# Kernel tuning notes

Hardware: AMD Instinct MI355X
Metric: run time of the kernel (lower is better)

The kernel has to match this reference:

```python
import jax, jax.numpy as jnp
import numpy as np

N_SAMPLES = 131072
N_FRAMES = 128
CPD = 16
WINDOW = 1024
N_VOICES = 8
N_BLOCKS = 3
N_CP = 512
N_VERBS = 8
MAX_ACTIVE = 32
BASE_RES = 0.5
MAX_GAIN = 5.0
B = 4
E = 16


def fft_convolve(a, b):
    # linear convolution via zero-padded rFFT, truncated to input length
    n = a.shape[-1]
    fa = jnp.fft.rfft(a, n=2 * n, axis=-1)
    fb = jnp.fft.rfft(b, n=2 * n, axis=-1)
    return jnp.fft.irfft(fa * fb, n=2 * n, axis=-1)[..., :n]


def sparsify(x, k):
    # keep top-k entries of the whole control plane, zero the rest
    flat = x.reshape(-1)
    vals, idx = jax.lax.top_k(flat, k)
    return jnp.zeros_like(flat).at[idx].set(vals).reshape(x.shape)


def run_layer(cp, w1, decays, w2, audio_map, gains):
    # cp: [CPD, F]
    frames = cp.shape[-1]
    x = w1 @ cp
    orig = x
    logd = jnp.log(1e-12 + decays)  # [CPD]
    env = jnp.exp(jnp.cumsum(jnp.broadcast_to(logd[:, None], (CPD, frames)), axis=-1))
    x = fft_convolve(x, env)
    x = w2 @ x + orig
    cp_out = jnp.tanh(x * gains[:, None])
    audio = (audio_map @ cp_out).T.reshape(-1)  # [F*WINDOW], frame-major
    return audio, cp_out


def stack_forward(cp, w1s, w2s, audios, decays_p, gains_p, mix):
    wc = cp
    outs = []
    for i in range(N_BLOCKS):
        d = BASE_RES + jax.nn.sigmoid(decays_p[i]) * (1.0 - BASE_RES)
        g = jax.nn.sigmoid(gains_p[i]) * MAX_GAIN
        out, wc = run_layer(jax.nn.relu(wc), w1s[i], d, w2s[i], audios[i], g)
        outs.append(out)
    channels = jnp.stack(outs, axis=0)  # [N_BLOCKS, N_SAMPLES]
    mixed = jnp.einsum('ct,c->t', channels, jax.nn.softmax(mix))
    return mixed / (jnp.max(jnp.abs(mixed)) + 1e-8)  # max_norm


def event_forward(voice_l, cp_choice, amp, room_l, room_mix_l, times,
                  cp_items, verbs, w1, w2, audio_maps, decays, gains, mix):
    vidx = jnp.argmax(voice_l)  # hard voice one-hot (normalize=True -> value 1.0)
    cp = cp_items[jnp.argmax(cp_choice)].reshape(CPD, N_FRAMES)
    cp = sparsify(cp / (cp.sum() + 1e-8), MAX_ACTIVE)
    samples = stack_forward(cp, w1[vidx], w2[vidx], audio_maps[vidx],
                            decays[vidx], gains[vidx], mix[vidx])  # [N_SAMPLES]
    verb = verbs[jnp.argmax(room_l)]  # hard reverb lookup
    wet = fft_convolve(verb, samples)
    vm = jax.nn.softmax(room_mix_l)  # [wet, dry]
    final = wet * vm[0] + samples * vm[1]
    final = final * jnp.abs(amp[0])
    # DiracScheduler: upsample-with-holes then FFT convolve
    step = N_SAMPLES // N_FRAMES
    impulse = jnp.zeros(N_SAMPLES, final.dtype).at[jnp.arange(N_FRAMES) * step].set(times)
    return fft_convolve(final, impulse)


def setup_inputs():
    key = jax.random.key(0)
    ks = jax.random.split(key, 14)
    return {
        'voice': jax.random.normal(ks[0], (B, E, N_VOICES), jnp.float32),
        'control_plane_choice': jax.random.normal(ks[1], (B, E, N_CP), jnp.float32),
        'amplitudes': jax.random.uniform(ks[2], (B, E, 1), jnp.float32),
        'room_choice': jax.random.normal(ks[3], (B, E, N_VERBS), jnp.float32),
        'room_mix': jax.random.normal(ks[4], (B, E, 2), jnp.float32),
        'times': jax.random.uniform(ks[5], (B, E, N_FRAMES), jnp.float32),
        'cp_items': jax.random.uniform(ks[6], (N_CP, N_FRAMES * CPD), jnp.float32),
        'verbs': jax.random.normal(ks[7], (N_VERBS, N_SAMPLES), jnp.float32) * 0.01,
        'w1': jax.random.normal(ks[8], (N_VOICES, N_BLOCKS, CPD, CPD), jnp.float32) * 0.01,
        'w2': jax.random.normal(ks[9], (N_VOICES, N_BLOCKS, CPD, CPD), jnp.float32) * 0.01,
        'audio_maps': jax.random.normal(ks[10], (N_VOICES, N_BLOCKS, WINDOW, CPD), jnp.float32) * 0.01,
        'decays': jax.random.normal(ks[11], (N_VOICES, N_BLOCKS, CPD), jnp.float32),
        'gains': jax.random.normal(ks[12], (N_VOICES, N_BLOCKS, CPD), jnp.float32),
        'mix': jax.random.normal(ks[13], (N_VOICES, N_BLOCKS), jnp.float32),
    }


def reference(voice, control_plane_choice, amplitudes, room_choice, room_mix, times,
              cp_items, verbs, w1, w2, audio_maps, decays, gains, mix):
    per_event = jax.vmap(jax.vmap(event_forward, in_axes=(0,) * 6 + (None,) * 8),
                         in_axes=(0,) * 6 + (None,) * 8)
    return per_event(voice, control_plane_choice, amplitudes, room_choice, room_mix, times,
                     cp_items, verbs, w1, w2, audio_maps, decays, gains, mix)
```

## Files before the change

### kernel.cpp

```cpp
#include <hip/hip_runtime.h>
#include <math.h>

#define NS 131072
#define NFR 128
#define CPDIM 16
#define WIN 1024
#define NVOICE 8
#define NBLK 3
#define NCP 512
#define NVERB 8
#define NEV 64
#define N1 1024
#define NBINS 1025
#define IDX(i) ((i) + ((i) >> 5))

struct EvParams {
  int vidx, cpidx, ridx;
  float vm0, vm1, amp;
  float mixw0, mixw1, mixw2;
  unsigned int maxslot;
  int pad[6];
};

__global__ void kt_tw(float2* __restrict__ tw) {
  int k = blockIdx.x * 256 + threadIdx.x;
  if (k < 1024) {
    float ang = -3.067961575771282340e-03f * (float)k;
    float s, c;
    sincosf(ang, &s, &c);
    tw[k] = make_float2(c, s);
  }
}

__device__ __forceinline__ void fft1024(float* re, float* im,
                                        const float* twr, const float* twi,
                                        int tid, bool inverse) {
  #pragma unroll
  for (int s = 1; s <= 10; ++s) {
    const int half = 1 << (s - 1);
    const int tsh = 11 - s;
    for (int k = tid; k < 512; k += 256) {
      int j = k & (half - 1);
      int i0 = ((k ^ j) << 1) | j;
      int i1 = IDX(i0 + half);
      i0 = IDX(i0);
      float wr = twr[j << tsh];
      float wi = twi[j << tsh];
      if (inverse) wi = -wi;
      float xr = re[i1], xi = im[i1];
      float tr = wr * xr - wi * xi;
      float ti = wr * xi + wi * xr;
      float ur = re[i0], ui = im[i0];
      re[i0] = ur + tr; im[i0] = ui + ti;
      re[i1] = ur - tr; im[i1] = ui - ti;
    }
    __syncthreads();
  }
}

__device__ __forceinline__ void rfft_fwd(const float2* __restrict__ src2, float scale,
                                         float2* __restrict__ dst,
                                         float* re, float* im, float* twr, float* twi,
                                         const float2* __restrict__ twg, int tid) {
  for (int i = tid; i < 1024; i += 256) { float2 w = twg[i]; twr[i] = w.x; twi[i] = w.y; }
  for (int n = tid; n < 1024; n += 256) {
    int r = IDX(__brev(n) >> 22);
    if (n < 512) {
      float2 x = src2[n];
      re[r] = x.x * scale; im[r] = x.y * scale;
    } else { re[r] = 0.0f; im[r] = 0.0f; }
  }
  __syncthreads();
  fft1024(re, im, twr, twi, tid, false);
  for (int k = tid; k <= 1024; k += 256) {
    int km = (1024 - k) & 1023;
    float zr = re[IDX(k & 1023)], zi = im[IDX(k & 1023)];
    float mr = re[IDX(km)], mi = im[IDX(km)];
    float Are = 0.5f * (zr + mr), Aim = 0.5f * (zi - mi);
    float Bre = 0.5f * (zi + mi), Bim = 0.5f * (mr - zr);
    float wr, wi;
    if (k == 1024) { wr = -1.0f; wi = 0.0f; }
    else { wr = twr[k]; wi = twi[k]; }
    dst[k] = make_float2(Are + wr * Bre - wi * Bim, Aim + wr * Bim + wi * Bre);
  }
}

__global__ void k0_params(const float* __restrict__ voice, const float* __restrict__ cpc,
                          const float* __restrict__ amps, const float* __restrict__ roomc,
                          const float* __restrict__ roomm, const float* __restrict__ mix,
                          EvParams* __restrict__ P) {
  int e = blockIdx.x;
  int tid = threadIdx.x;
  __shared__ float bvals[64];
  __shared__ int bidx[64];

  if (tid == 0) {
    const float* v = voice + e * NVOICE;
    int vi = 0; float bv = v[0];
    for (int i = 1; i < NVOICE; ++i) if (v[i] > bv) { bv = v[i]; vi = i; }
    P[e].vidx = vi;

    const float* r = roomc + e * NVERB;
    int ri = 0; float br = r[0];
    for (int i = 1; i < NVERB; ++i) if (r[i] > br) { br = r[i]; ri = i; }
    P[e].ridx = ri;

    float m0 = roomm[e * 2 + 0], m1 = roomm[e * 2 + 1];
    float mx = fmaxf(m0, m1);
    float e0 = expf(m0 - mx), e1 = expf(m1 - mx);
    float inv = 1.0f / (e0 + e1);
    P[e].vm0 = e0 * inv;
    P[e].vm1 = e1 * inv;
    P[e].amp = fabsf(amps[e]);

    const float* mm = mix + vi * NBLK;
    float mmx = fmaxf(fmaxf(mm[0], mm[1]), mm[2]);
    float w0 = expf(mm[0] - mmx), w1 = expf(mm[1] - mmx), w2 = expf(mm[2] - mmx);
    float si = 1.0f / (w0 + w1 + w2);
    P[e].mixw0 = w0 * si; P[e].mixw1 = w1 * si; P[e].mixw2 = w2 * si;
    P[e].maxslot = 0u;
  }

  const float* c = cpc + (size_t)e * NCP;
  float bv = -INFINITY; int bi = 0;
  for (int i = tid; i < NCP; i += 64) {
    float x = c[i];
    if (x > bv) { bv = x; bi = i; }
  }
  bvals[tid] = bv; bidx[tid] = bi;
  __syncthreads();
  if (tid == 0) {
    float best = bvals[0]; int besti = bidx[0];
    for (int i = 1; i < 64; ++i) {
      if (bvals[i] > best || (bvals[i] == best && bidx[i] < besti)) { best = bvals[i]; besti = bidx[i]; }
    }
    P[e].cpidx = besti;
  }
}

__global__ __launch_bounds__(256) void kv_fft(const float* __restrict__ verbs,
                                              const float2* __restrict__ twg,
                                              float2* __restrict__ Vhat) {
  __shared__ float re[N1 + 32], im[N1 + 32];
  __shared__ float twr[N1], twi[N1];
  int v = blockIdx.x >> 7, j = blockIdx.x & 127;
  int tid = threadIdx.x;
  rfft_fwd((const float2*)(verbs + (size_t)v * NS + j * WIN), 1.0f,
           Vhat + ((size_t)v * NFR + j) * NBINS, re, im, twr, twi, twg, tid);
}

__global__ __launch_bounds__(256) void k1a_synth(const float* __restrict__ cp_items,
                                                 const float* __restrict__ w1_all,
                                                 const float* __restrict__ w2_all,
                                                 const float* __restrict__ decays,
                                                 const float* __restrict__ gains,
                                                 const EvParams* __restrict__ P,
                                                 float* __restrict__ cp_out_all) {
  __shared__ float wc[2048], xb[2048], yb[2048];
  __shared__ float w1s[256], w2s[256];
  __shared__ float dv[16], gv[16];
  __shared__ float rv[4];
  __shared__ int ri[4];
  __shared__ float s_scale;

  int e = blockIdx.x, tid = threadIdx.x;
  int vidx = P[e].vidx, cpidx = P[e].cpidx;
  int base = tid * 8;

  float vals[8];
  float ls = 0.0f;
  #pragma unroll
  for (int q = 0; q < 8; ++q) {
    float x = cp_items[(size_t)cpidx * 2048 + base + q];
    vals[q] = x; ls += x;
  }
  #pragma unroll
  for (int off = 32; off > 0; off >>= 1) ls += __shfl_xor(ls, off);
  if ((tid & 63) == 0) rv[tid >> 6] = ls;
  __syncthreads();
  if (tid == 0) s_scale = 1.0f / (rv[0] + rv[1] + rv[2] + rv[3] + 1e-8f);
  for (int i = tid; i < 2048; i += 256) wc[i] = 0.0f;
  __syncthreads();
  float scale = s_scale;

  for (int it = 0; it < 32; ++it) {
    float bv = -1.0f; int bi = 1 << 30;
    #pragma unroll
    for (int q = 0; q < 8; ++q) {
      if (vals[q] > bv) { bv = vals[q]; bi = base + q; }
    }
    #pragma unroll
    for (int off = 32; off > 0; off >>= 1) {
      float ov = __shfl_xor(bv, off); int oi = __shfl_xor(bi, off);
      if (ov > bv || (ov == bv && oi < bi)) { bv = ov; bi = oi; }
    }
    if ((tid & 63) == 0) { rv[tid >> 6] = bv; ri[tid >> 6] = bi; }
    __syncthreads();
    float wv = rv[0]; int wi = ri[0];
    #pragma unroll
    for (int w = 1; w < 4; ++w) {
      if (rv[w] > wv || (rv[w] == wv && ri[w] < wi)) { wv = rv[w]; wi = ri[w]; }
    }
    if ((wi >> 3) == tid) { vals[wi & 7] = -2.0f; wc[wi] = wv * scale; }
    __syncthreads();
  }

  for (int l = 0; l < NBLK; ++l) {
    int wbase = (vidx * NBLK + l) * 256;
    w1s[tid] = w1_all[wbase + tid];
    w2s[tid] = w2_all[wbase + tid];
    if (tid < 16) {
      float dp = decays[(vidx * NBLK + l) * 16 + tid];
      float sd = 1.0f / (1.0f + expf(-dp));
      dv[tid] = 1e-12f + 0.5f + 0.5f * sd;
      float gp = gains[(vidx * NBLK + l) * 16 + tid];
      gv[tid] = 5.0f / (1.0f + expf(-gp));
    }
    __syncthreads();
    for (int i = tid; i < 2048; i += 256) {
      int cch = i >> 7, f = i & 127;
      float acc = 0.0f;
      #pragma unroll
      for (int k = 0; k < 16; ++k) acc += w1s[cch * 16 + k] * fmaxf(wc[k * 128 + f], 0.0f);
      xb[i] = acc;
    }
    __syncthreads();
    if (tid < 16) {
      float a = 0.0f, d = dv[tid];
      for (int t = 0; t < 128; ++t) { a = d * (a + xb[tid * 128 + t]); yb[tid * 128 + t] = a; }
    }
    __syncthreads();
    for (int i = tid; i < 2048; i += 256) {
      int cch = i >> 7, f = i & 127;
      float acc = xb[i];
      #pragma unroll
      for (int k = 0; k < 16; ++k) acc += w2s[cch * 16 + k] * yb[k * 128 + f];
      float co = tanhf(acc * gv[cch]);
      wc[i] = co;
      cp_out_all[((size_t)e * NBLK + l) * 2048 + i] = co;
    }
    __syncthreads();
  }
}

__global__ __launch_bounds__(256) void k1b_audio(const float* __restrict__ amaps,
                                                 const float* __restrict__ cp_out_all,
                                                 EvParams* __restrict__ P,
                                                 float* __restrict__ mixed) {
  __shared__ float cps[NBLK][16][16];
  __shared__ float red[256];
  int e = blockIdx.x >> 3, fg = blockIdx.x & 7;
  int f0 = fg * 16, tid = threadIdx.x;
  int vidx = P[e].vidx;
  float mw[3] = {P[e].mixw0, P[e].mixw1, P[e].mixw2};

  for (int i = tid; i < NBLK * 256; i += 256) {
    int bl = i >> 8, r = i & 255, cch = r >> 4, fl = r & 15;
    cps[bl][cch][fl] = cp_out_all[((size_t)e * NBLK + bl) * 2048 + cch * 128 + f0 + fl];
  }
  __syncthreads();

  float amax = 0.0f;
  for (int jw = 0; jw < 4; ++jw) {
    int w = jw * 256 + tid;
    float am[NBLK][16];
    #pragma unroll
    for (int bl = 0; bl < NBLK; ++bl) {
      const float* ap = amaps + (((size_t)(vidx * NBLK + bl)) * WIN + w) * CPDIM;
      #pragma unroll
      for (int cch = 0; cch < 16; ++cch) am[bl][cch] = ap[cch] * mw[bl];
    }
    for (int fl = 0; fl < 16; ++fl) {
      float acc = 0.0f;
      #pragma unroll
      for (int bl = 0; bl < NBLK; ++bl)
        #pragma unroll
        for (int cch = 0; cch < 16; ++cch) acc += am[bl][cch] * cps[bl][cch][fl];
      mixed[(size_t)e * NS + (size_t)(f0 + fl) * WIN + w] = acc;
      amax = fmaxf(amax, fabsf(acc));
    }
  }
  red[tid] = amax;
  __syncthreads();
  for (int s = 128; s > 0; s >>= 1) { if (tid < s) red[tid] = fmaxf(red[tid], red[tid + s]); __syncthreads(); }
  if (tid == 0) atomicMax(&P[e].maxslot, __float_as_uint(red[0]));
}

__global__ __launch_bounds__(256) void k2_fwd(const float* __restrict__ mixed,
                                              const float2* __restrict__ twg,
                                              float2* __restrict__ Shat) {
  __shared__ float re[N1 + 32], im[N1 + 32];
  __shared__ float twr[N1], twi[N1];
  int e = blockIdx.x >> 7, p = blockIdx.x & 127;
  int tid = threadIdx.x;
  rfft_fwd((const float2*)(mixed + (size_t)e * NS + p * WIN), 1.0f,
           Shat + ((size_t)e * NFR + p) * NBINS, re, im, twr, twi, twg, tid);
}

__global__ __launch_bounds__(256, 4) void k3_conv(const float2* __restrict__ Shat,
                                                  const float2* __restrict__ Vhat,
                                                  const float* __restrict__ times_g,
                                                  const EvParams* __restrict__ P,
                                                  float2* __restrict__ Ohat) {
  __shared__ float2 S2[128 * 17];
  __shared__ float2 V2[128 * 17];
  __shared__ float tms[128];

  int bx = blockIdx.x;
  int e = bx / 65, bg = bx % 65;
  int bin0 = bg * 16;
  int tid = threadIdx.x;
  int b = tid & 15, pg = tid >> 4;
  int p0 = pg * 8;

  int ridx = P[e].ridx;
  float vm0 = P[e].vm0, vm1 = P[e].vm1;
  float amp = P[e].amp / (__uint_as_float(P[e].maxslot) + 1e-8f);

  const float2* Sg = Shat + (size_t)e * NFR * NBINS;
  const float2* Vg = Vhat + (size_t)ridx * NFR * NBINS;
  for (int i = tid; i < 2048; i += 256) {
    int f = i >> 4, bb = i & 15;
    int bin = bin0 + bb; if (bin > 1024) bin = 1024;
    S2[f * 17 + bb] = Sg[f * NBINS + bin];
    V2[f * 17 + bb] = Vg[f * NBINS + bin];
  }
  if (tid < 128) tms[tid] = times_g[e * NFR + tid];
  __syncthreads();

  float ar[8], ai[8];
  #pragma unroll
  for (int t = 0; t < 8; ++t) { ar[t] = 0.0f; ai[t] = 0.0f; }

  for (int ft = 0; ft < pg; ++ft) {
    int f0v = ft * 8;
    float2 s[8];
    #pragma unroll
    for (int ff = 0; ff < 8; ++ff) s[ff] = S2[(f0v + ff) * 17 + b];
    float2 v[15];
    int jb = p0 - f0v - 7;
    #pragma unroll
    for (int m = 0; m < 15; ++m) v[m] = V2[(jb + m) * 17 + b];
    #pragma unroll
    for (int ff = 0; ff < 8; ++ff) {
      #pragma unroll
      for (int t = 0; t < 8; ++t) {
        int m = 7 - ff + t;
        ar[t] += s[ff].x * v[m].x - s[ff].y * v[m].y;
        ai[t] += s[ff].x * v[m].y + s[ff].y * v[m].x;
      }
    }
  }
  {
    float2 s[8];
    #pragma unroll
    for (int ff = 0; ff < 8; ++ff) s[ff] = S2[(p0 + ff) * 17 + b];
    float2 v[8];
    #pragma unroll
    for (int m = 0; m < 8; ++m) v[m] = V2[m * 17 + b];
    #pragma unroll
    for (int ff = 0; ff < 8; ++ff) {
      #pragma unroll
      for (int t = 0; t < 8; ++t) {
        if (t >= ff) {
          int m = t - ff;
          ar[t] += s[ff].x * v[m].x - s[ff].y * v[m].y;
          ai[t] += s[ff].x * v[m].y + s[ff].y * v[m].x;
        }
      }
    }
  }

  __syncthreads();
  #pragma unroll
  for (int t = 0; t < 8; ++t) {
    int p = p0 + t;
    float2 sv = S2[p * 17 + b];
    V2[p * 17 + b] = make_float2(amp * (vm0 * ar[t] + vm1 * sv.x),
                                 amp * (vm0 * ai[t] + vm1 * sv.y));
  }
  __syncthreads();

  #pragma unroll
  for (int t = 0; t < 8; ++t) { ar[t] = 0.0f; ai[t] = 0.0f; }

  for (int ft = 0; ft < pg; ++ft) {
    int f0v = ft * 8;
    float trr[8];
    #pragma unroll
    for (int ff = 0; ff < 8; ++ff) trr[ff] = tms[f0v + ff];
    float2 u[15];
    int jb = p0 - f0v - 7;
    #pragma unroll
    for (int m = 0; m < 15; ++m) u[m] = V2[(jb + m) * 17 + b];
    #pragma unroll
    for (int ff = 0; ff < 8; ++ff) {
      #pragma unroll
      for (int t = 0; t < 8; ++t) {
        int m = 7 - ff + t;
        ar[t] += trr[ff] * u[m].x;
        ai[t] += trr[ff] * u[m].y;
      }
    }
  }
  {
    float trr[8];
    #pragma unroll
    for (int ff = 0; ff < 8; ++ff) trr[ff] = tms[p0 + ff];
    float2 u[8];
    #pragma unroll
    for (int m = 0; m < 8; ++m) u[m] = V2[m * 17 + b];
    #pragma unroll
    for (int ff = 0; ff < 8; ++ff) {
      #pragma unroll
      for (int t = 0; t < 8; ++t) {
        if (t >= ff) {
          int m = t - ff;
          ar[t] += trr[ff] * u[m].x;
          ai[t] += trr[ff] * u[m].y;
        }
      }
    }
  }

  int bin = bin0 + b;
  if (bin <= 1024) {
    float2* Og = Ohat + (size_t)e * NFR * NBINS;
    #pragma unroll
    for (int t = 0; t < 8; ++t) {
      Og[(p0 + t) * NBINS + bin] = make_float2(ar[t], ai[t]);
    }
  }
}

__global__ __launch_bounds__(256) void k4_ifft(const float2* __restrict__ Ohat,
                                               const float2* __restrict__ twg,
                                               float* __restrict__ out,
                                               float* __restrict__ tail) {
  __shared__ float re[N1 + 32], im[N1 + 32];
  __shared__ float twr[N1], twi[N1];
  int e = blockIdx.x >> 7, p = blockIdx.x & 127;
  int tid = threadIdx.x;
  const float2* src = Ohat + ((size_t)e * NFR + p) * NBINS;
  for (int i = tid; i < 1024; i += 256) { float2 w = twg[i]; twr[i] = w.x; twi[i] = w.y; }
  __syncthreads();
  for (int k = tid; k < 1024; k += 256) {
    float2 Xk = src[k];
    float2 Xm = src[1024 - k];
    float Are = 0.5f * (Xk.x + Xm.x), Aim = 0.5f * (Xk.y - Xm.y);
    float Dre = 0.5f * (Xk.x - Xm.x), Dim = 0.5f * (Xk.y + Xm.y);
    float wr = twr[k], wi = twi[k];
    float Bre = wr * Dre + wi * Dim;
    float Bim = wr * Dim - wi * Dre;
    int r = IDX(__brev(k) >> 22);
    re[r] = Are - Bim;
    im[r] = Aim + Bre;
  }
  __syncthreads();
  fft1024(re, im, twr, twi, tid, true);
  const float inv = 1.0f / (float)N1;
  float2* o2 = (float2*)(out + (size_t)e * NS + (size_t)p * WIN);
  for (int n = tid; n < 512; n += 256) o2[n] = make_float2(re[IDX(n)] * inv, im[IDX(n)] * inv);
  float2* t2 = (float2*)(tail + ((size_t)e * NFR + p) * WIN);
  for (int n = tid; n < 512; n += 256) t2[n] = make_float2(re[IDX(n + 512)] * inv, im[IDX(n + 512)] * inv);
}

__global__ __launch_bounds__(256) void k5_tail(const float* __restrict__ tail, float* __restrict__ out) {
  size_t idx = (size_t)blockIdx.x * 256 + threadIdx.x;
  if (idx >= (size_t)NEV * 127 * WIN) return;
  int u = (int)(idx & 1023);
  size_t rest = idx >> 10;
  int pm1 = (int)(rest % 127);
  int e = (int)(rest / 127);
  int p = pm1 + 1;
  out[(size_t)e * NS + (size_t)p * WIN + u] += tail[((size_t)e * NFR + pm1) * WIN + u];
}

extern "C" void kernel_launch(void* const* d_in, const int* in_sizes, int n_in,
                              void* d_out, int out_size, void* d_ws, size_t ws_size,
                              hipStream_t stream) {
  (void)in_sizes; (void)n_in; (void)out_size; (void)ws_size;
  const float* voice    = (const float*)d_in[0];
  const float* cpc      = (const float*)d_in[1];
  const float* amps     = (const float*)d_in[2];
  const float* roomc    = (const float*)d_in[3];
  const float* roomm    = (const float*)d_in[4];
  const float* times    = (const float*)d_in[5];
  const float* cp_items = (const float*)d_in[6];
  const float* verbs    = (const float*)d_in[7];
  const float* w1       = (const float*)d_in[8];
  const float* w2       = (const float*)d_in[9];
  const float* amaps    = (const float*)d_in[10];
  const float* decays   = (const float*)d_in[11];
  const float* gains    = (const float*)d_in[12];
  const float* mix      = (const float*)d_in[13];
  float* out = (float*)d_out;

  char* base = (char*)d_ws;
  EvParams* P       = (EvParams*)base;
  float2* twg       = (float2*)(base + 4096);
  float* cp_out_all = (float*)(base + 4096 + 8192);
  float* mixed      = cp_out_all + (size_t)393216;
  float2* Shat      = (float2*)(mixed + (size_t)8388608);
  float2* Vhat      = Shat + (size_t)NEV * NFR * NBINS;
  float* tail  = mixed;
  float2* Ohat = Shat;

  kt_tw<<<4, 256, 0, stream>>>(twg);
  k0_params<<<NEV, 64, 0, stream>>>(voice, cpc, amps, roomc, roomm, mix, P);
  kv_fft<<<NVERB * NFR, 256, 0, stream>>>(verbs, twg, Vhat);
  k1a_synth<<<NEV, 256, 0, stream>>>(cp_items, w1, w2, decays, gains, P, cp_out_all);
  k1b_audio<<<NEV * 8, 256, 0, stream>>>(amaps, cp_out_all, P, mixed);
  k2_fwd<<<NEV * NFR, 256, 0, stream>>>(mixed, twg, Shat);
  k3_conv<<<NEV * 65, 256, 0, stream>>>(Shat, Vhat, times, P, Ohat);
  k4_ifft<<<NEV * NFR, 256, 0, stream>>>(Ohat, twg, out, tail);
  k5_tail<<<(NEV * 127 * WIN) / 256, 256, 0, stream>>>(tail, out);
}
```

Before: 690.2 us.

## Replace direct frame-axis block convolution with 512-point FFT along frame dimension

New measurement: 672.9 us. -2.5%, faster.

```diff
diff --git a/kernel.cpp b/kernel.cpp
--- a/kernel.cpp
+++ b/kernel.cpp
@@ -13,6 +13,7 @@
 #define N1 1024
 #define NBINS 1025
 #define IDX(i) ((i) + ((i) >> 5))
+#define VT_MAIN_BINS 1016
 
 struct EvParams {
   int vidx, cpidx, ridx;
@@ -85,6 +86,58 @@
   }
 }
 
+template<int NROWS>
+__device__ __forceinline__ void fft512_rows(float* re, float* im,
+                                            const float* twr, const float* twi,
+                                            int tid) {
+  #pragma unroll
+  for (int s = 1; s <= 9; ++s) {
+    const int half = 1 << (s - 1);
+    const int tsh = 9 - s;
+    for (int q = tid; q < NROWS * 256; q += 256) {
+      int row = q >> 8, k = q & 255;
+      int j = k & (half - 1);
+      int i0 = ((k ^ j) << 1) | j;
+      int a0 = row * 513 + i0, a1 = a0 + half;
+      float wr = twr[j << tsh];
+      float wi = twi[j << tsh];
+      float xr = re[a1], xi = im[a1];
+      float tr = wr * xr - wi * xi;
+      float ti = wr * xi + wi * xr;
+      float ur = re[a0], ui = im[a0];
+      re[a0] = ur + tr; im[a0] = ui + ti;
+      re[a1] = ur - tr; im[a1] = ui - ti;
+    }
+    __syncthreads();
+  }
+}
+
+template<int NROWS>
+__device__ __forceinline__ void ifft512_rows_dif(float* re, float* im,
+                                                 const float* twr, const float* twi,
+                                                 int tid) {
+  #pragma unroll
+  for (int s = 9; s >= 1; --s) {
+    const int half = 1 << (s - 1);
+    const int tsh = 9 - s;
+    for (int q = tid; q < NROWS * 256; q += 256) {
+      int row = q >> 8, k = q & 255;
+      int j = k & (half - 1);
+      int i0 = ((k ^ j) << 1) | j;
+      int a0 = row * 513 + i0, a1 = a0 + half;
+      float wr = twr[j << tsh];
+      float wi = -twi[j << tsh];
+      float ur = re[a0], ui = im[a0];
+      float vr = re[a1], vi = im[a1];
+      re[a0] = ur + vr; im[a0] = ui + vi;
+      float dr = ur - vr, di = ui - vi;
+      re[a1] = dr * wr - di * wi;
+      im[a1] = dr * wi + di * wr;
+    }
+    __syncthreads();
+  }
+}
+
 __global__ void k0_params(const float* __restrict__ voice, const float* __restrict__ cpc,
                           const float* __restrict__ amps, const float* __restrict__ roomc,
                           const float* __restrict__ roomm, const float* __restrict__ mix,
@@ -147,6 +200,59 @@
   int tid = threadIdx.x;
   rfft_fwd((const float2*)(verbs + (size_t)v * NS + j * WIN), 1.0f,
            Vhat + ((size_t)v * NFR + j) * NBINS, re, im, twr, twi, twg, tid);
+}
+
+__global__ __launch_bounds__(256) void kv2_cfft(const float2* __restrict__ Vhat,
+                                                const float2* __restrict__ twg,
+                                                float2* __restrict__ VtMain,
+                                                float2* __restrict__ VtRest) {
+  __shared__ float zre[8 * 513], zim[8 * 513];
+  __shared__ float twr[256], twi[256];
+  int v = blockIdx.x / 129, bg = blockIdx.x % 129;
+  int b0 = bg * 8;
+  int tid = threadIdx.x;
+  { float2 w = twg[4 * tid]; twr[tid] = w.x; twi[tid] = w.y; }
+  const float2* Vg = Vhat + (size_t)v * NFR * NBINS;
+  for (int idx = tid; idx < 1024; idx += 256) {
+    int p = idx >> 3, bb = idx & 7;
+    int bin = b0 + bb; if (bin > 1024) bin = 1024;
+    float2 x = Vg[p * NBINS + bin];
+    int r = __brev(p) >> 23;
+    zre[bb * 513 + r] = x.x; zim[bb * 513 + r] = x.y;
+  }
+  for (int idx = tid; idx < 3072; idx += 256) {
+    int p = 128 + (idx >> 3), bb = idx & 7;
+    int r = __brev(p) >> 23;
+    zre[bb * 513 + r] = 0.f; zim[bb * 513 + r] = 0.f;
+  }
+  __syncthreads();
+  fft512_rows<8>(zre, zim, twr, twi, tid);
+  for (int idx = tid; idx < 4096; idx += 256) {
+    int bb = idx >> 9, c = idx & 511;
+    int bin = b0 + bb;
+    if (bin <= 1024) {
+      float2 val = make_float2(zre[bb * 513 + c], zim[bb * 513 + c]);
+      if (bin < VT_MAIN_BINS) VtMain[((size_t)v * VT_MAIN_BINS + bin) * 512 + c] = val;
+      else VtRest[((size_t)v * 9 + (bin - VT_MAIN_BINS)) * 512 + c] = val;
+    }
+  }
+}
+
+__global__ __launch_bounds__(256) void kt_times(const float* __restrict__ times_g,
+                                                const float2* __restrict__ twg,
+                                                float2* __restrict__ That) {
+  __shared__ float re[513], im[513];
+  __shared__ float twr[256], twi[256];
+  int e = blockIdx.x, tid = threadIdx.x;
+  { float2 w = twg[4 * tid]; twr[tid] = w.x; twi[tid] = w.y; }
+  for (int p = tid; p < 512; p += 256) {
+    int r = __brev(p) >> 23;
+    float v = (p < 128) ? times_g[e * NFR + p] : 0.f;
+    re[r] = v; im[r] = 0.f;
+  }
+  __syncthreads();
+  fft512_rows<1>(re, im, twr, twi, tid);
+  for (int c = tid; c < 512; c += 256) That[(size_t)e * 512 + c] = make_float2(re[c], im[c]);
 }
 
 __global__ __launch_bounds__(256) void k1a_synth(const float* __restrict__ cp_items,
@@ -297,139 +403,59 @@
            Shat + ((size_t)e * NFR + p) * NBINS, re, im, twr, twi, twg, tid);
 }
 
-__global__ __launch_bounds__(256, 4) void k3_conv(const float2* __restrict__ Shat,
-                                                  const float2* __restrict__ Vhat,
-                                                  const float* __restrict__ times_g,
-                                                  const EvParams* __restrict__ P,
-                                                  float2* __restrict__ Ohat) {
-  __shared__ float2 S2[128 * 17];
-  __shared__ float2 V2[128 * 17];
-  __shared__ float tms[128];
-
-  int bx = blockIdx.x;
-  int e = bx / 65, bg = bx % 65;
-  int bin0 = bg * 16;
+__global__ __launch_bounds__(256) void k3_fft(float2* __restrict__ Shat,
+                                              const float2* __restrict__ VtMain,
+                                              const float2* __restrict__ VtRest,
+                                              const float2* __restrict__ That,
+                                              const float2* __restrict__ twg,
+                                              const EvParams* __restrict__ P) {
+  __shared__ float zre[8 * 513], zim[8 * 513];
+  __shared__ float twr[256], twi[256];
+  int e = blockIdx.x / 129, bg = blockIdx.x % 129;
+  int b0 = bg * 8;
   int tid = threadIdx.x;
-  int b = tid & 15, pg = tid >> 4;
-  int p0 = pg * 8;
-
   int ridx = P[e].ridx;
   float vm0 = P[e].vm0, vm1 = P[e].vm1;
-  float amp = P[e].amp / (__uint_as_float(P[e].maxslot) + 1e-8f);
-
-  const float2* Sg = Shat + (size_t)e * NFR * NBINS;
-  const float2* Vg = Vhat + (size_t)ridx * NFR * NBINS;
-  for (int i = tid; i < 2048; i += 256) {
-    int f = i >> 4, bb = i & 15;
-    int bin = bin0 + bb; if (bin > 1024) bin = 1024;
-    S2[f * 17 + bb] = Sg[f * NBINS + bin];
-    V2[f * 17 + bb] = Vg[f * NBINS + bin];
-  }
-  if (tid < 128) tms[tid] = times_g[e * NFR + tid];
-  __syncthreads();
-
-  float ar[8], ai[8];
-  #pragma unroll
-  for (int t = 0; t < 8; ++t) { ar[t] = 0.0f; ai[t] = 0.0f; }
-
-  for (int ft = 0; ft < pg; ++ft) {
-    int f0v = ft * 8;
-    float2 s[8];
-    #pragma unroll
-    for (int ff = 0; ff < 8; ++ff) s[ff] = S2[(f0v + ff) * 17 + b];
-    float2 v[15];
-    int jb = p0 - f0v - 7;
-    #pragma unroll
-    for (int m = 0; m < 15; ++m) v[m] = V2[(jb + m) * 17 + b];
-    #pragma unroll
-    for (int ff = 0; ff < 8; ++ff) {
-      #pragma unroll
-      for (int t = 0; t < 8; ++t) {
-        int m = 7 - ff + t;
-        ar[t] += s[ff].x * v[m].x - s[ff].y * v[m].y;
-        ai[t] += s[ff].x * v[m].y + s[ff].y * v[m].x;
-      }
-    }
-  }
-  {
-    float2 s[8];
-    #pragma unroll
-    for (int ff = 0; ff < 8; ++ff) s[ff] = S2[(p0 + ff) * 17 + b];
-    float2 v[8];
-    #pragma unroll
-    for (int m = 0; m < 8; ++m) v[m] = V2[m * 17 + b];
-    #pragma unroll
-    for (int ff = 0; ff < 8; ++ff) {
-      #pragma unroll
-      for (int t = 0; t < 8; ++t) {
-        if (t >= ff) {
-          int m = t - ff;
-          ar[t] += s[ff].x * v[m].x - s[ff].y * v[m].y;
-          ai[t] += s[ff].x * v[m].y + s[ff].y * v[m].x;
-        }
-      }
-    }
-  }
-
-  __syncthreads();
-  #pragma unroll
-  for (int t = 0; t < 8; ++t) {
-    int p = p0 + t;
-    float2 sv = S2[p * 17 + b];
-    V2[p * 17 + b] = make_float2(amp * (vm0 * ar[t] + vm1 * sv.x),
-                                 amp * (vm0 * ai[t] + vm1 * sv.y));
-  }
-  __syncthreads();
-
-  #pragma unroll
-  for (int t = 0; t < 8; ++t) { ar[t] = 0.0f; ai[t] = 0.0f; }
-
-  for (int ft = 0; ft < pg; ++ft) {
-    int f0v = ft * 8;
-    float trr[8];
-    #pragma unroll
-    for (int ff = 0; ff < 8; ++ff) trr[ff] = tms[f0v + ff];
-    float2 u[15];
-    int jb = p0 - f0v - 7;
-    #pragma unroll
-    for (int m = 0; m < 15; ++m) u[m] = V2[(jb + m) * 17 + b];
-    #pragma unroll
-    for (int ff = 0; ff < 8; ++ff) {
-      #pragma unroll
-      for (int t = 0; t < 8; ++t) {
-        int m = 7 - ff + t;
-        ar[t] += trr[ff] * u[m].x;
-        ai[t] += trr[ff] * u[m].y;
-      }
-    }
-  }
-  {
-    float trr[8];
-    #pragma unroll
-    for (int ff = 0; ff < 8; ++ff) trr[ff] = tms[p0 + ff];
-    float2 u[8];
-    #pragma unroll
-    for (int m = 0; m < 8; ++m) u[m] = V2[m * 17 + b];
-    #pragma unroll
-    for (int ff = 0; ff < 8; ++ff) {
-      #pragma unroll
-      for (int t = 0; t < 8; ++t) {
-        if (t >= ff) {
-          int m = t - ff;
-          ar[t] += trr[ff] * u[m].x;
-          ai[t] += trr[ff] * u[m].y;
-        }
-      }
-    }
-  }
-
-  int bin = bin0 + b;
-  if (bin <= 1024) {
-    float2* Og = Ohat + (size_t)e * NFR * NBINS;
-    #pragma unroll
-    for (int t = 0; t < 8; ++t) {
-      Og[(p0 + t) * NBINS + bin] = make_float2(ar[t], ai[t]);
-    }
+  float ampn = P[e].amp / (__uint_as_float(P[e].maxslot) + 1e-8f) * (1.0f / 512.0f);
+  { float2 w = twg[4 * tid]; twr[tid] = w.x; twi[tid] = w.y; }
+
+  float2* Sg = Shat + (size_t)e * NFR * NBINS;
+  for (int idx = tid; idx < 1024; idx += 256) {
+    int p = idx >> 3, bb = idx & 7;
+    int bin = b0 + bb; if (bin > 1024) bin = 1024;
+    float2 x = Sg[p * NBINS + bin];
+    int r = __brev(p) >> 23;
+    zre[bb * 513 + r] = x.x; zim[bb * 513 + r] = x.y;
+  }
+  for (int idx = tid; idx < 3072; idx += 256) {
+    int p = 128 + (idx >> 3), bb = idx & 7;
+    int r = __brev(p) >> 23;
+    zre[bb * 513 + r] = 0.f; zim[bb * 513 + r] = 0.f;
+  }
+  __syncthreads();
+  fft512_rows<8>(zre, zim, twr, twi, tid);
+
+  for (int idx = tid; idx < 4096; idx += 256) {
+    int bb = idx >> 9, c = idx & 511;
+    int bin = b0 + bb; if (bin > 1024) bin = 1024;
+    float2 V = (bin < VT_MAIN_BINS) ? VtMain[((size_t)ridx * VT_MAIN_BINS + bin) * 512 + c]
+                                    : VtRest[((size_t)ridx * 9 + (bin - VT_MAIN_BINS)) * 512 + c];
+    float2 T = That[(size_t)e * 512 + c];
+    float wr0 = vm0 * V.x + vm1, wi0 = vm0 * V.y;
+    float wr = (wr0 * T.x - wi0 * T.y) * ampn;
+    float wi = (wr0 * T.y + wi0 * T.x) * ampn;
+    float zr = zre[bb * 513 + c], zi = zim[bb * 513 + c];
+    zre[bb * 513 + c] = zr * wr - zi * wi;
+    zim[bb * 513 + c] = zr * wi + zi * wr;
+  }
+  __syncthreads();
+  ifft512_rows_dif<8>(zre, zim, twr, twi, tid);
+
+  for (int idx = tid; idx < 1024; idx += 256) {
+    int p = idx >> 3, bb = idx & 7;
+    int bin = b0 + bb;
+    int r = __brev(p) >> 23;
+    if (bin <= 1024) Sg[p * NBINS + bin] = make_float2(zre[bb * 513 + r], zim[bb * 513 + r]);
   }
 }
 
@@ -503,6 +529,9 @@
   float* mixed      = cp_out_all + (size_t)393216;
   float2* Shat      = (float2*)(mixed + (size_t)8388608);
   float2* Vhat      = Shat + (size_t)NEV * NFR * NBINS;
+  float2* That      = (float2*)cp_out_all;
+  float2* VtRest    = (float2*)((char*)cp_out_all + 262144);
+  float2* VtMain    = (float2*)out;
   float* tail  = mixed;
   float2* Ohat = Shat;
 
@@ -511,8 +540,10 @@
   kv_fft<<<NVERB * NFR, 256, 0, stream>>>(verbs, twg, Vhat);
   k1a_synth<<<NEV, 256, 0, stream>>>(cp_items, w1, w2, decays, gains, P, cp_out_all);
   k1b_audio<<<NEV * 8, 256, 0, stream>>>(amaps, cp_out_all, P, mixed);
+  kv2_cfft<<<NVERB * 129, 256, 0, stream>>>(Vhat, twg, VtMain, VtRest);
+  kt_times<<<NEV, 256, 0, stream>>>(times, twg, That);
   k2_fwd<<<NEV * NFR, 256, 0, stream>>>(mixed, twg, Shat);
-  k3_conv<<<NEV * 65, 256, 0, stream>>>(Shat, Vhat, times, P, Ohat);
+  k3_fft<<<NEV * 129, 256, 0, stream>>>(Shat, VtMain, VtRest, That, twg, P);
   k4_ifft<<<NEV * NFR, 256, 0, stream>>>(Ohat, twg, out, tail);
   k5_tail<<<(NEV * 127 * WIN) / 256, 256, 0, stream>>>(tail, out);
 }
```
